# Kernel tuning notes

Measured on AMD Instinct MI355X. Metric: run time of the kernel, lower is better.

## Reference

```python
import jax, jax.numpy as jnp
import numpy as np

N = 50000
E = 800000
D_IN = 128
D_OUT = 128
K = 3


def setup_inputs() -> dict:
    key = jax.random.key(0)
    k1, k2, k3, k4, k5 = jax.random.split(key, 5)
    x = jax.random.normal(k1, (N, D_IN), dtype=jnp.float32)
    TT = jax.random.uniform(k2, (E, K), dtype=jnp.float32)
    weight = jax.random.normal(k3, (D_IN, D_OUT, K), dtype=jnp.float32) * 0.1
    bias = jax.random.normal(k4, (D_OUT,), dtype=jnp.float32) * 0.1
    edge_idx = jax.random.randint(k5, (2, E), 0, N, dtype=jnp.int64)
    return {"x": x, "TT": TT, "weight": weight, "bias": bias, "edge_idx": edge_idx}


def reference(x, TT, weight, bias, edge_idx):
    # out = sum_k A_k @ (x @ W[:, :, k]) + bias, A_k sparse COO with values TT[:, k]
    n = x.shape[0]
    row, col = edge_idx[0], edge_idx[1]
    out = jnp.zeros((n, weight.shape[1]), dtype=x.dtype)
    for k in range(weight.shape[2]):  # small fixed kernel count
        support = x @ weight[:, :, k]                 # [N, out]
        msg = TT[:, k, None] * support[col]           # [E, out] gather + scale
        out = out + jax.ops.segment_sum(msg, row, num_segments=n)
    return out + bias
```

## Files before the change

kernel.cpp:

```cpp
#include <hip/hip_runtime.h>
#include <hip/hip_fp16.h>

#define DIM 128
#define KK 3
#define RPB 16
#define ZPAD 392
#define EBLK 4096
#define NBKT 256
#define CAPB 5120
#define QF   512
#define OVF_CAP 65536

typedef __attribute__((ext_vector_type(4))) float f32x4;
typedef __attribute__((ext_vector_type(8))) short bf16x8;

__device__ __forceinline__ unsigned pkbf(float lo, float hi) {
    unsigned a = __float_as_uint(lo), b = __float_as_uint(hi);
    a = (a + 0x7fffu + ((a >> 16) & 1u)) >> 16;
    b = (b + 0x7fffu + ((b >> 16) & 1u)) & 0xffff0000u;
    return (a & 0xffffu) | b;
}

__global__ __launch_bounds__(256) void k1a_kernel(
        const float* __restrict__ x, const float* __restrict__ w,
        uint2* __restrict__ xb2q, bf16x8* __restrict__ wbf,
        int xq_total, int xblk) {
    int b = blockIdx.x;
    if (b < xblk) {
        int i = b * 256 + threadIdx.x;
        if (i < xq_total) {
            float4 v = ((const float4*)x)[i];
            xb2q[i] = make_uint2(pkbf(v.x, v.y), pkbf(v.z, v.w));
        }
    } else {
        int t = (b - xblk) * 256 + threadIdx.x;
        if (t < 12 * 8 * 64) {
            int lane = t & 63;
            int quad = lane >> 4;
            int nn = ((t >> 6) & 7) * 16 + (lane & 15);
            int kbase = (t >> 9) * 32 + quad * 8;
            short vals[8];
#pragma unroll
            for (int j = 0; j < 8; ++j) {
                int k = kbase + j;
                int k3 = k >> 7, i2 = k & (DIM - 1);
                unsigned bv = __float_as_uint(w[((size_t)i2 * DIM + nn) * KK + k3]);
                vals[j] = (short)((bv + 0x7fffu + ((bv >> 16) & 1u)) >> 16);
            }
            wbf[t] = *(const bf16x8*)vals;
        }
    }
}

__global__ __launch_bounds__(1024) void binA_kernel(
        const float* __restrict__ TT, const int* __restrict__ eidx,
        int* __restrict__ bucketCnt, uint4* __restrict__ rec16,
        int* __restrict__ ovf_cnt, uint4* __restrict__ ovf, int E) {
    __shared__ unsigned sw0[EBLK], sw1[EBLK], sw2[EBLK], sw3[EBLK];
    __shared__ int hist[NBKT], scn[NBKT], cursor[NBKT], gbase[NBKT];
    int tid = threadIdx.x, blk = blockIdx.x;
    int e0 = blk * EBLK;
    int nval = min(EBLK, E - e0);

    if (tid < NBKT) hist[tid] = 0;
    __syncthreads();

    unsigned w0v[4], w1v[4], w2v[4], w3v[4];
    int bv[4];
#pragma unroll
    for (int i = 0; i < 4; ++i) {
        int li = tid + i * 1024;
        bv[i] = -1;
        if (li < nval) {
            int e = e0 + li;
            int row = eidx[e];
            int col = eidx[(size_t)E + e];
            w0v[i] = (unsigned)col | ((unsigned)row << 16);
            w1v[i] = __float_as_uint(TT[(size_t)e * 3 + 0]);
            w2v[i] = __float_as_uint(TT[(size_t)e * 3 + 1]);
            w3v[i] = __float_as_uint(TT[(size_t)e * 3 + 2]);
            bv[i] = row >> 8;
            atomicAdd(&hist[bv[i]], 1);
        }
    }
    __syncthreads();

    if (tid < NBKT) scn[tid] = hist[tid];
    __syncthreads();
    for (int d = 1; d < NBKT; d <<= 1) {
        int v = 0;
        if (tid < NBKT && tid >= d) v = scn[tid - d];
        __syncthreads();
        if (tid < NBKT && tid >= d) scn[tid] += v;
        __syncthreads();
    }
    if (tid < NBKT) {
        int ex = scn[tid] - hist[tid];
        scn[tid] = ex;
        cursor[tid] = ex;
        gbase[tid] = atomicAdd(&bucketCnt[tid], hist[tid]);
    }
    __syncthreads();

#pragma unroll
    for (int i = 0; i < 4; ++i) {
        if (bv[i] >= 0) {
            int lpos = atomicAdd(&cursor[bv[i]], 1);
            sw0[lpos] = w0v[i]; sw1[lpos] = w1v[i];
            sw2[lpos] = w2v[i]; sw3[lpos] = w3v[i];
        }
    }
    __syncthreads();

    for (int s = tid; s < nval; s += 1024) {
        unsigned u0 = sw0[s];
        int bb = (int)(u0 >> 24);
        int gpos = gbase[bb] + (s - scn[bb]);
        if (gpos < CAPB) {
            rec16[(size_t)bb * CAPB + gpos] = make_uint4(u0, sw1[s], sw2[s], sw3[s]);
        } else {
            int op = atomicAdd(ovf_cnt, 1);
            if (op < OVF_CAP)
                ovf[op] = make_uint4(u0, sw1[s], sw2[s], sw3[s]);
        }
    }
}

__global__ __launch_bounds__(1024) void binB_kernel(
        const uint4* __restrict__ rec16, const int* __restrict__ bucketCnt,
        uint4* __restrict__ out16, int* __restrict__ rowStart,
        int* __restrict__ rowCnt) {
    __shared__ uint4 ostage[CAPB];
    __shared__ int hist[256], scn[256], cursor[256];
    int b = blockIdx.x, tid = threadIdx.x;
    int cntb = min(bucketCnt[b], CAPB);

    if (tid < 256) hist[tid] = 0;
    __syncthreads();
    for (int i = tid; i < cntb; i += 1024) {
        unsigned u0 = rec16[(size_t)b * CAPB + i].x;
        atomicAdd(&hist[(u0 >> 16) & 255u], 1);
    }
    __syncthreads();
    if (tid < 256) scn[tid] = hist[tid];
    __syncthreads();
    for (int d = 1; d < 256; d <<= 1) {
        int v = 0;
        if (tid < 256 && tid >= d) v = scn[tid - d];
        __syncthreads();
        if (tid < 256 && tid >= d) scn[tid] += v;
        __syncthreads();
    }
    if (tid < 256) {
        int ex = scn[tid] - hist[tid];
        scn[tid] = ex;
        cursor[tid] = ex;
        rowStart[b * 256 + tid] = b * CAPB + ex;
        rowCnt[b * 256 + tid] = hist[tid];
    }
    __syncthreads();
    for (int i = tid; i < cntb; i += 1024) {
        uint4 r = rec16[(size_t)b * CAPB + i];
        int rl = (int)((r.x >> 16) & 255u);
        int pos = atomicAdd(&cursor[rl], 1);
        ostage[pos] = r;
    }
    __syncthreads();
    for (int i = tid; i < cntb; i += 1024)
        out16[(size_t)b * CAPB + i] = ostage[i];
}

__device__ __forceinline__ void edge_fma(uint4 rc, const unsigned* __restrict__ xb2, int lane,
        float& a0l, float& a0h, float& a1l, float& a1h, float& a2l, float& a2h) {
    int c = rc.x & 0xffffu;
    float t0 = __uint_as_float(rc.y);
    float t1 = __uint_as_float(rc.z);
    float t2 = __uint_as_float(rc.w);
    unsigned u = xb2[(size_t)c * 64 + lane];
    float xl = __uint_as_float(u << 16), xh = __uint_as_float(u & 0xffff0000u);
    a0l = fmaf(t0, xl, a0l); a0h = fmaf(t0, xh, a0h);
    a1l = fmaf(t1, xl, a1l); a1h = fmaf(t1, xh, a1h);
    a2l = fmaf(t2, xl, a2l); a2h = fmaf(t2, xh, a2h);
}

__global__ __launch_bounds__(256) void fused_kernel(const uint4* __restrict__ out16,
        const int* __restrict__ rowStart, const int* __restrict__ rowCnt,
        const unsigned* __restrict__ xb2, const bf16x8* __restrict__ wbf,
        const float* __restrict__ bias, float* __restrict__ out, int n) {
    __shared__ short zs16[RPB][ZPAD];
    __shared__ uint4 qflat[QF];
    __shared__ int rs[RPB], rc[RPB];
    int tid = threadIdx.x;
    int lane = tid & 63, wv = tid >> 6;
    int n0 = blockIdx.x * RPB;

    if (tid < RPB) {
        int r = n0 + tid;
        rs[tid] = (r < n) ? rowStart[r] : 0;
        rc[tid] = (r < n) ? rowCnt[r] : 0;
    }
    __syncthreads();
    int base = rs[0];
    int tot = rs[RPB - 1] + rc[RPB - 1] - base;

    float A[4][6];
#pragma unroll
    for (int ii = 0; ii < 4; ++ii)
#pragma unroll
        for (int j = 0; j < 6; ++j) A[ii][j] = 0.f;

    for (int c0 = 0; c0 < tot; c0 += QF) {
        int cl = min(QF, tot - c0);
        __syncthreads();
        for (int i = tid; i < cl; i += 256) qflat[i] = out16[(size_t)base + c0 + i];
        __syncthreads();
#pragma unroll
        for (int ii = 0; ii < 4; ++ii) {
            int rl = wv * 4 + ii;
            int s = rs[rl] - base, e = s + rc[rl];
            int lo = max(s, c0), hi = min(e, c0 + cl);
            int p = lo;
            for (; p + 8 <= hi; p += 8) {
#pragma unroll
                for (int u8 = 0; u8 < 8; ++u8)
                    edge_fma(qflat[p - c0 + u8], xb2, lane,
                             A[ii][0], A[ii][1], A[ii][2], A[ii][3], A[ii][4], A[ii][5]);
            }
            for (; p + 4 <= hi; p += 4) {
#pragma unroll
                for (int u4 = 0; u4 < 4; ++u4)
                    edge_fma(qflat[p - c0 + u4], xb2, lane,
                             A[ii][0], A[ii][1], A[ii][2], A[ii][3], A[ii][4], A[ii][5]);
            }
            for (; p < hi; ++p)
                edge_fma(qflat[p - c0], xb2, lane,
                         A[ii][0], A[ii][1], A[ii][2], A[ii][3], A[ii][4], A[ii][5]);
        }
    }

#pragma unroll
    for (int ii = 0; ii < 4; ++ii) {
        int rl = wv * 4 + ii;
        *(unsigned*)&zs16[rl][0 * DIM + 2 * lane] = pkbf(A[ii][0], A[ii][1]);
        *(unsigned*)&zs16[rl][1 * DIM + 2 * lane] = pkbf(A[ii][2], A[ii][3]);
        *(unsigned*)&zs16[rl][2 * DIM + 2 * lane] = pkbf(A[ii][4], A[ii][5]);
    }
    __syncthreads();

    int quad = lane >> 4, m = lane & 15;
    int nt0 = wv * 2, nt1 = wv * 2 + 1;
    f32x4 acc0 = {0.f, 0.f, 0.f, 0.f}, acc1 = {0.f, 0.f, 0.f, 0.f};
#pragma unroll
    for (int kt = 0; kt < 12; ++kt) {
        bf16x8 a  = *(const bf16x8*)&zs16[m][kt * 32 + quad * 8];
        bf16x8 b0 = wbf[(kt * 8 + nt0) * 64 + lane];
        bf16x8 b1 = wbf[(kt * 8 + nt1) * 64 + lane];
        acc0 = __builtin_amdgcn_mfma_f32_16x16x32_bf16(a, b0, acc0, 0, 0, 0);
        acc1 = __builtin_amdgcn_mfma_f32_16x16x32_bf16(a, b1, acc1, 0, 0, 0);
    }
    float bi0 = bias[nt0 * 16 + m], bi1 = bias[nt1 * 16 + m];
#pragma unroll
    for (int rr = 0; rr < 4; ++rr) {
        int node = n0 + quad * 4 + rr;
        if (node < n) {
            out[(size_t)node * DIM + nt0 * 16 + m] = acc0[rr] + bi0;
            out[(size_t)node * DIM + nt1 * 16 + m] = acc1[rr] + bi1;
        }
    }
}

__global__ __launch_bounds__(128) void ovf_kernel(const uint4* __restrict__ ovf,
        const int* __restrict__ ovf_cnt, const float* __restrict__ x,
        const float* __restrict__ w, float* __restrict__ out) {
    int total = min(*ovf_cnt, OVF_CAP);
    int d = threadIdx.x;
    for (int i = blockIdx.x; i < total; i += gridDim.x) {
        uint4 r = ovf[i];
        int col = (int)(r.x & 0xffffu), row = (int)(r.x >> 16);
        float t0 = __uint_as_float(r.y);
        float t1 = __uint_as_float(r.z);
        float t2 = __uint_as_float(r.w);
        float acc = 0.f;
        for (int ii = 0; ii < DIM; ++ii) {
            const float* wp = &w[((size_t)ii * DIM + d) * KK];
            acc = fmaf(x[(size_t)col * DIM + ii],
                       t0 * wp[0] + t1 * wp[1] + t2 * wp[2], acc);
        }
        atomicAdd(&out[(size_t)row * DIM + d], acc);
    }
}

extern "C" void kernel_launch(void* const* d_in, const int* in_sizes, int n_in,
                              void* d_out, int out_size, void* d_ws, size_t ws_size,
                              hipStream_t stream) {
    const float* x    = (const float*)d_in[0];
    const float* TT   = (const float*)d_in[1];
    const float* w    = (const float*)d_in[2];
    const float* bias = (const float*)d_in[3];
    const int*   eidx = (const int*)d_in[4];
    float* out = (float*)d_out;

    int n = in_sizes[0] / DIM;
    int E = in_sizes[1] / KK;
    int nbkt = (n + 255) >> 8;

    char* ws = (char*)d_ws;
    size_t o = 0;
    auto take = [&](size_t b) { void* p = ws + o; o += (b + 255) & ~(size_t)255; return p; };
    uint4*    rec16 = (uint4*)take((size_t)nbkt * CAPB * 16);
    uint4*    out16 = (uint4*)take((size_t)nbkt * CAPB * 16);
    int*      rowStart = (int*)take((size_t)nbkt * 256 * 4);
    int*      rowCnt   = (int*)take((size_t)nbkt * 256 * 4);
    int*      bcnt  = (int*)take((size_t)(NBKT + 64) * 4);
    uint4*    ovf   = (uint4*)take((size_t)OVF_CAP * 16);
    bf16x8*   wbf   = (bf16x8*)take((size_t)12 * 8 * 64 * 16);
    unsigned* xb2   = (unsigned*)take((size_t)n * DIM * 2);
    (void)ws_size;
    int* ovf_cnt = bcnt + NBKT;

    hipMemsetAsync(bcnt, 0, (size_t)(NBKT + 64) * 4, stream);

    int xq = n * DIM / 4;
    int xblk = (xq + 255) / 256;
    int ablk = (E + EBLK - 1) / EBLK;

    k1a_kernel<<<xblk + 24, 256, 0, stream>>>(x, w, (uint2*)xb2, wbf, xq, xblk);
    binA_kernel<<<ablk, 1024, 0, stream>>>(TT, eidx, bcnt, rec16, ovf_cnt, ovf, E);
    binB_kernel<<<nbkt, 1024, 0, stream>>>(rec16, bcnt, out16, rowStart, rowCnt);
    fused_kernel<<<(n + RPB - 1) / RPB, 256, 0, stream>>>(
        out16, rowStart, rowCnt, xb2, wbf, bias, out, n);
    ovf_kernel<<<64, 128, 0, stream>>>(ovf, ovf_cnt, x, w, out);
}
```

Measured before the change: 164.1 us.

## Split binB per bucket quarter and make fused kernel persistent with prefetch

binB now launches four blocks per bucket. Each block handles a quarter of the rows, which halves the shared staging buffer and raises parallelism. The fused kernel becomes persistent with a fixed grid, each block processing up to four 16-row tiles. It double-buffers the edge-record loads by prefetching the next tile's records into registers while the current tile is gathered and multiplied. Tiles with more than QF edges now spill their extra records to the overflow path instead of looping, which adds atomics and leaves correctness dependent on the overflow kernel.

```diff
diff --git a/kernel.cpp b/kernel.cpp
--- a/kernel.cpp
+++ b/kernel.cpp
@@ -9,6 +9,9 @@
 #define NBKT 256
 #define CAPB 5120
 #define QF   512
+#define CAPQ 2560
+#define TPB  4
+#define FGRID 1024
 #define OVF_CAP 65536
 
 typedef __attribute__((ext_vector_type(4))) float f32x4;
@@ -130,15 +133,15 @@
         const uint4* __restrict__ rec16, const int* __restrict__ bucketCnt,
         uint4* __restrict__ out16, int* __restrict__ rowStart,
         int* __restrict__ rowCnt) {
-    __shared__ uint4 ostage[CAPB];
-    __shared__ int hist[256], scn[256], cursor[256];
-    int b = blockIdx.x, tid = threadIdx.x;
-    int cntb = min(bucketCnt[b], CAPB);
+    __shared__ uint4 ostage[CAPQ];
+    __shared__ int hist[256], scn[256], cursor[64];
+    int bb = blockIdx.x >> 2, q = blockIdx.x & 3, tid = threadIdx.x;
+    int cntb = min(bucketCnt[bb], CAPB);
 
     if (tid < 256) hist[tid] = 0;
     __syncthreads();
     for (int i = tid; i < cntb; i += 1024) {
-        unsigned u0 = rec16[(size_t)b * CAPB + i].x;
+        unsigned u0 = rec16[(size_t)bb * CAPB + i].x;
         atomicAdd(&hist[(u0 >> 16) & 255u], 1);
     }
     __syncthreads();
@@ -151,23 +154,32 @@
         if (tid < 256 && tid >= d) scn[tid] += v;
         __syncthreads();
     }
+    int r0 = q * 64;
     if (tid < 256) {
         int ex = scn[tid] - hist[tid];
         scn[tid] = ex;
-        cursor[tid] = ex;
-        rowStart[b * 256 + tid] = b * CAPB + ex;
-        rowCnt[b * 256 + tid] = hist[tid];
-    }
+        if ((tid >> 6) == q) {
+            rowStart[bb * 256 + tid] = bb * CAPB + ex;
+            rowCnt[bb * 256 + tid] = hist[tid];
+        }
+    }
+    __syncthreads();
+    int qbase = scn[r0];
+    int qend = (q == 3) ? cntb : scn[r0 + 64];
+    if (tid < 64) cursor[tid] = scn[r0 + tid] - qbase;
     __syncthreads();
     for (int i = tid; i < cntb; i += 1024) {
-        uint4 r = rec16[(size_t)b * CAPB + i];
-        int rl = (int)((r.x >> 16) & 255u);
-        int pos = atomicAdd(&cursor[rl], 1);
-        ostage[pos] = r;
-    }
-    __syncthreads();
-    for (int i = tid; i < cntb; i += 1024)
-        out16[(size_t)b * CAPB + i] = ostage[i];
+        uint4 r = rec16[(size_t)bb * CAPB + i];
+        int rr = (int)((r.x >> 16) & 255u);
+        if ((rr >> 6) == q) {
+            int pos = atomicAdd(&cursor[rr - r0], 1);
+            if (pos < CAPQ) ostage[pos] = r;
+        }
+    }
+    __syncthreads();
+    int qcnt = min(qend - qbase, CAPQ);
+    for (int i = tid; i < qcnt; i += 1024)
+        out16[(size_t)bb * CAPB + qbase + i] = ostage[i];
 }
 
 __device__ __forceinline__ void edge_fma(uint4 rc, const unsigned* __restrict__ xb2, int lane,
@@ -186,86 +198,116 @@
 __global__ __launch_bounds__(256) void fused_kernel(const uint4* __restrict__ out16,
         const int* __restrict__ rowStart, const int* __restrict__ rowCnt,
         const unsigned* __restrict__ xb2, const bf16x8* __restrict__ wbf,
-        const float* __restrict__ bias, float* __restrict__ out, int n) {
+        const float* __restrict__ bias, float* __restrict__ out,
+        int* __restrict__ ovf_cnt, uint4* __restrict__ ovf,
+        int n, int ntiles) {
     __shared__ short zs16[RPB][ZPAD];
-    __shared__ uint4 qflat[QF];
-    __shared__ int rs[RPB], rc[RPB];
+    __shared__ uint4 qbuf[2][QF];
+    __shared__ int rsL[TPB][RPB], rcL[TPB][RPB];
     int tid = threadIdx.x;
     int lane = tid & 63, wv = tid >> 6;
-    int n0 = blockIdx.x * RPB;
+    int bid = blockIdx.x;
 
     if (tid < RPB) {
-        int r = n0 + tid;
-        rs[tid] = (r < n) ? rowStart[r] : 0;
-        rc[tid] = (r < n) ? rowCnt[r] : 0;
-    }
-    __syncthreads();
-    int base = rs[0];
-    int tot = rs[RPB - 1] + rc[RPB - 1] - base;
-
-    float A[4][6];
-#pragma unroll
-    for (int ii = 0; ii < 4; ++ii)
-#pragma unroll
-        for (int j = 0; j < 6; ++j) A[ii][j] = 0.f;
-
-    for (int c0 = 0; c0 < tot; c0 += QF) {
-        int cl = min(QF, tot - c0);
-        __syncthreads();
-        for (int i = tid; i < cl; i += 256) qflat[i] = out16[(size_t)base + c0 + i];
-        __syncthreads();
+#pragma unroll
+        for (int k = 0; k < TPB; ++k) {
+            int tt = bid + k * FGRID;
+            if (tt < ntiles) {
+                int r = tt * RPB + tid;
+                rsL[k][tid] = (r < n) ? rowStart[r] : 0;
+                rcL[k][tid] = (r < n) ? rowCnt[r] : 0;
+            }
+        }
+    }
+    __syncthreads();
+
+    {
+        int base0 = rsL[0][0];
+        int raw0 = rsL[0][RPB - 1] + rcL[0][RPB - 1] - base0;
+        for (int i = tid; i < raw0; i += 256) {
+            uint4 r = out16[(size_t)base0 + i];
+            if (i < QF) qbuf[0][i] = r;
+            else {
+                int op = atomicAdd(ovf_cnt, 1);
+                if (op < OVF_CAP) ovf[op] = r;
+            }
+        }
+    }
+    __syncthreads();
+
+    int quad = lane >> 4, m = lane & 15;
+    int nt0 = wv * 2, nt1 = wv * 2 + 1;
+    float bi0 = bias[nt0 * 16 + m], bi1 = bias[nt1 * 16 + m];
+    int buf = 0;
+
+    for (int k = 0; k < TPB && (bid + k * FGRID) < ntiles; ++k) {
+        int n0 = (bid + k * FGRID) * RPB;
+        int base = rsL[k][0];
+
+        bool hasn = (k + 1 < TPB) && (bid + (k + 1) * FGRID) < ntiles;
+        uint4 pf0, pf1; int ntot = 0;
+        if (hasn) {
+            int nbase = rsL[k + 1][0];
+            int rawn = rsL[k + 1][RPB - 1] + rcL[k + 1][RPB - 1] - nbase;
+            ntot = min(rawn, QF);
+            if (tid < ntot) pf0 = out16[(size_t)nbase + tid];
+            if (256 + tid < ntot) pf1 = out16[(size_t)nbase + 256 + tid];
+            for (int i = QF + tid; i < rawn; i += 256) {
+                int op = atomicAdd(ovf_cnt, 1);
+                if (op < OVF_CAP) ovf[op] = out16[(size_t)nbase + i];
+            }
+        }
+
+        const uint4* qf = qbuf[buf];
 #pragma unroll
         for (int ii = 0; ii < 4; ++ii) {
             int rl = wv * 4 + ii;
-            int s = rs[rl] - base, e = s + rc[rl];
-            int lo = max(s, c0), hi = min(e, c0 + cl);
-            int p = lo;
-            for (; p + 8 <= hi; p += 8) {
-#pragma unroll
-                for (int u8 = 0; u8 < 8; ++u8)
-                    edge_fma(qflat[p - c0 + u8], xb2, lane,
-                             A[ii][0], A[ii][1], A[ii][2], A[ii][3], A[ii][4], A[ii][5]);
+            float a0l = 0, a0h = 0, a1l = 0, a1h = 0, a2l = 0, a2h = 0;
+            int s = rsL[k][rl] - base;
+            int hi = min(s + rcL[k][rl], QF);
+            int p = min(s, QF);
+            for (; p + 16 <= hi; p += 16) {
+#pragma unroll
+                for (int u = 0; u < 16; ++u)
+                    edge_fma(qf[p + u], xb2, lane, a0l, a0h, a1l, a1h, a2l, a2h);
             }
             for (; p + 4 <= hi; p += 4) {
 #pragma unroll
-                for (int u4 = 0; u4 < 4; ++u4)
-                    edge_fma(qflat[p - c0 + u4], xb2, lane,
-                             A[ii][0], A[ii][1], A[ii][2], A[ii][3], A[ii][4], A[ii][5]);
+                for (int u = 0; u < 4; ++u)
+                    edge_fma(qf[p + u], xb2, lane, a0l, a0h, a1l, a1h, a2l, a2h);
             }
             for (; p < hi; ++p)
-                edge_fma(qflat[p - c0], xb2, lane,
-                         A[ii][0], A[ii][1], A[ii][2], A[ii][3], A[ii][4], A[ii][5]);
-        }
-    }
-
-#pragma unroll
-    for (int ii = 0; ii < 4; ++ii) {
-        int rl = wv * 4 + ii;
-        *(unsigned*)&zs16[rl][0 * DIM + 2 * lane] = pkbf(A[ii][0], A[ii][1]);
-        *(unsigned*)&zs16[rl][1 * DIM + 2 * lane] = pkbf(A[ii][2], A[ii][3]);
-        *(unsigned*)&zs16[rl][2 * DIM + 2 * lane] = pkbf(A[ii][4], A[ii][5]);
-    }
-    __syncthreads();
-
-    int quad = lane >> 4, m = lane & 15;
-    int nt0 = wv * 2, nt1 = wv * 2 + 1;
-    f32x4 acc0 = {0.f, 0.f, 0.f, 0.f}, acc1 = {0.f, 0.f, 0.f, 0.f};
-#pragma unroll
-    for (int kt = 0; kt < 12; ++kt) {
-        bf16x8 a  = *(const bf16x8*)&zs16[m][kt * 32 + quad * 8];
-        bf16x8 b0 = wbf[(kt * 8 + nt0) * 64 + lane];
-        bf16x8 b1 = wbf[(kt * 8 + nt1) * 64 + lane];
-        acc0 = __builtin_amdgcn_mfma_f32_16x16x32_bf16(a, b0, acc0, 0, 0, 0);
-        acc1 = __builtin_amdgcn_mfma_f32_16x16x32_bf16(a, b1, acc1, 0, 0, 0);
-    }
-    float bi0 = bias[nt0 * 16 + m], bi1 = bias[nt1 * 16 + m];
-#pragma unroll
-    for (int rr = 0; rr < 4; ++rr) {
-        int node = n0 + quad * 4 + rr;
-        if (node < n) {
-            out[(size_t)node * DIM + nt0 * 16 + m] = acc0[rr] + bi0;
-            out[(size_t)node * DIM + nt1 * 16 + m] = acc1[rr] + bi1;
-        }
+                edge_fma(qf[p], xb2, lane, a0l, a0h, a1l, a1h, a2l, a2h);
+            *(unsigned*)&zs16[rl][0 * DIM + 2 * lane] = pkbf(a0l, a0h);
+            *(unsigned*)&zs16[rl][1 * DIM + 2 * lane] = pkbf(a1l, a1h);
+            *(unsigned*)&zs16[rl][2 * DIM + 2 * lane] = pkbf(a2l, a2h);
+        }
+        __syncthreads();
+
+        f32x4 acc0 = {0.f, 0.f, 0.f, 0.f}, acc1 = {0.f, 0.f, 0.f, 0.f};
+#pragma unroll
+        for (int kt = 0; kt < 12; ++kt) {
+            bf16x8 a  = *(const bf16x8*)&zs16[m][kt * 32 + quad * 8];
+            bf16x8 b0 = wbf[(kt * 8 + nt0) * 64 + lane];
+            bf16x8 b1 = wbf[(kt * 8 + nt1) * 64 + lane];
+            acc0 = __builtin_amdgcn_mfma_f32_16x16x32_bf16(a, b0, acc0, 0, 0, 0);
+            acc1 = __builtin_amdgcn_mfma_f32_16x16x32_bf16(a, b1, acc1, 0, 0, 0);
+        }
+#pragma unroll
+        for (int rr = 0; rr < 4; ++rr) {
+            int node = n0 + quad * 4 + rr;
+            if (node < n) {
+                out[(size_t)node * DIM + nt0 * 16 + m] = acc0[rr] + bi0;
+                out[(size_t)node * DIM + nt1 * 16 + m] = acc1[rr] + bi1;
+            }
+        }
+
+        if (hasn) {
+            if (tid < ntot) qbuf[buf ^ 1][tid] = pf0;
+            if (256 + tid < ntot) qbuf[buf ^ 1][256 + tid] = pf1;
+        }
+        __syncthreads();
+        buf ^= 1;
     }
 }
 
@@ -303,12 +345,13 @@
     int n = in_sizes[0] / DIM;
     int E = in_sizes[1] / KK;
     int nbkt = (n + 255) >> 8;
+    int ntiles = (n + RPB - 1) / RPB;
 
     char* ws = (char*)d_ws;
     size_t o = 0;
     auto take = [&](size_t b) { void* p = ws + o; o += (b + 255) & ~(size_t)255; return p; };
     uint4*    rec16 = (uint4*)take((size_t)nbkt * CAPB * 16);
-    uint4*    out16 = (uint4*)take((size_t)nbkt * CAPB * 16);
+    uint4*    out16 = (uint4*)take((size_t)nbkt * CAPB * 16 + 8192);
     int*      rowStart = (int*)take((size_t)nbkt * 256 * 4);
     int*      rowCnt   = (int*)take((size_t)nbkt * 256 * 4);
     int*      bcnt  = (int*)take((size_t)(NBKT + 64) * 4);
@@ -326,8 +369,8 @@
 
     k1a_kernel<<<xblk + 24, 256, 0, stream>>>(x, w, (uint2*)xb2, wbf, xq, xblk);
     binA_kernel<<<ablk, 1024, 0, stream>>>(TT, eidx, bcnt, rec16, ovf_cnt, ovf, E);
-    binB_kernel<<<nbkt, 1024, 0, stream>>>(rec16, bcnt, out16, rowStart, rowCnt);
-    fused_kernel<<<(n + RPB - 1) / RPB, 256, 0, stream>>>(
-        out16, rowStart, rowCnt, xb2, wbf, bias, out, n);
+    binB_kernel<<<nbkt * 4, 1024, 0, stream>>>(rec16, bcnt, out16, rowStart, rowCnt);
+    fused_kernel<<<FGRID, 256, 0, stream>>>(
+        out16, rowStart, rowCnt, xb2, wbf, bias, out, ovf_cnt, ovf, n, ntiles);
     ovf_kernel<<<64, 128, 0, stream>>>(ovf, ovf_cnt, x, w, out);
 }
```

Result: slower. 244.9 us (+49.2%).

## Merge prep and binning kernels; single-chunk gather with overflow spill in fused kernel

Applied to the files above, without the earlier changes.

Folds the bf16 conversion, weight packing and edge-binning (binA) work into one 1024-thread launch, which removes a kernel launch and its boundary. The fused kernel now stages at most QF edge records per 16-row tile in shared memory. Any excess records are pushed to the global overflow list with an atomic, so ovf_kernel handles them instead of running a multi-chunk loop. This makes the gather loop simpler, but the x/w conversion blocks now carry the large shared-memory footprint of the binning path, which may reduce their occupancy. Correctness also depends on the overflow buffer being large enough.

```diff
diff --git a/kernel.cpp b/kernel.cpp
--- a/kernel.cpp
+++ b/kernel.cpp
@@ -21,19 +21,27 @@
     return (a & 0xffffu) | b;
 }
 
-__global__ __launch_bounds__(256) void k1a_kernel(
+__global__ __launch_bounds__(1024) void prep_kernel(
         const float* __restrict__ x, const float* __restrict__ w,
+        const float* __restrict__ TT, const int* __restrict__ eidx,
         uint2* __restrict__ xb2q, bf16x8* __restrict__ wbf,
-        int xq_total, int xblk) {
-    int b = blockIdx.x;
+        int* __restrict__ bucketCnt, uint4* __restrict__ rec16,
+        int* __restrict__ ovf_cnt, uint4* __restrict__ ovf,
+        int xq_total, int xblk, int E) {
+    __shared__ unsigned sw0[EBLK], sw1[EBLK], sw2[EBLK], sw3[EBLK];
+    __shared__ int hist[NBKT], scn[NBKT], cursor[NBKT], gbase[NBKT];
+    int tid = threadIdx.x, b = blockIdx.x;
+
     if (b < xblk) {
-        int i = b * 256 + threadIdx.x;
+        int i = b * 1024 + tid;
         if (i < xq_total) {
             float4 v = ((const float4*)x)[i];
             xb2q[i] = make_uint2(pkbf(v.x, v.y), pkbf(v.z, v.w));
         }
-    } else {
-        int t = (b - xblk) * 256 + threadIdx.x;
+        return;
+    }
+    if (b < xblk + 6) {
+        int t = (b - xblk) * 1024 + tid;
         if (t < 12 * 8 * 64) {
             int lane = t & 63;
             int quad = lane >> 4;
@@ -49,17 +57,10 @@
             }
             wbf[t] = *(const bf16x8*)vals;
         }
-    }
-}
-
-__global__ __launch_bounds__(1024) void binA_kernel(
-        const float* __restrict__ TT, const int* __restrict__ eidx,
-        int* __restrict__ bucketCnt, uint4* __restrict__ rec16,
-        int* __restrict__ ovf_cnt, uint4* __restrict__ ovf, int E) {
-    __shared__ unsigned sw0[EBLK], sw1[EBLK], sw2[EBLK], sw3[EBLK];
-    __shared__ int hist[NBKT], scn[NBKT], cursor[NBKT], gbase[NBKT];
-    int tid = threadIdx.x, blk = blockIdx.x;
-    int e0 = blk * EBLK;
+        return;
+    }
+
+    int e0 = (b - xblk - 6) * EBLK;
     int nval = min(EBLK, E - e0);
 
     if (tid < NBKT) hist[tid] = 0;
@@ -186,7 +187,8 @@
 __global__ __launch_bounds__(256) void fused_kernel(const uint4* __restrict__ out16,
         const int* __restrict__ rowStart, const int* __restrict__ rowCnt,
         const unsigned* __restrict__ xb2, const bf16x8* __restrict__ wbf,
-        const float* __restrict__ bias, float* __restrict__ out, int n) {
+        const float* __restrict__ bias, float* __restrict__ out,
+        int* __restrict__ ovf_cnt, uint4* __restrict__ ovf, int n) {
     __shared__ short zs16[RPB][ZPAD];
     __shared__ uint4 qflat[QF];
     __shared__ int rs[RPB], rc[RPB];
@@ -203,47 +205,35 @@
     int base = rs[0];
     int tot = rs[RPB - 1] + rc[RPB - 1] - base;
 
-    float A[4][6];
-#pragma unroll
-    for (int ii = 0; ii < 4; ++ii)
-#pragma unroll
-        for (int j = 0; j < 6; ++j) A[ii][j] = 0.f;
-
-    for (int c0 = 0; c0 < tot; c0 += QF) {
-        int cl = min(QF, tot - c0);
-        __syncthreads();
-        for (int i = tid; i < cl; i += 256) qflat[i] = out16[(size_t)base + c0 + i];
-        __syncthreads();
-#pragma unroll
-        for (int ii = 0; ii < 4; ++ii) {
-            int rl = wv * 4 + ii;
-            int s = rs[rl] - base, e = s + rc[rl];
-            int lo = max(s, c0), hi = min(e, c0 + cl);
-            int p = lo;
-            for (; p + 8 <= hi; p += 8) {
-#pragma unroll
-                for (int u8 = 0; u8 < 8; ++u8)
-                    edge_fma(qflat[p - c0 + u8], xb2, lane,
-                             A[ii][0], A[ii][1], A[ii][2], A[ii][3], A[ii][4], A[ii][5]);
-            }
-            for (; p + 4 <= hi; p += 4) {
-#pragma unroll
-                for (int u4 = 0; u4 < 4; ++u4)
-                    edge_fma(qflat[p - c0 + u4], xb2, lane,
-                             A[ii][0], A[ii][1], A[ii][2], A[ii][3], A[ii][4], A[ii][5]);
-            }
-            for (; p < hi; ++p)
-                edge_fma(qflat[p - c0], xb2, lane,
-                         A[ii][0], A[ii][1], A[ii][2], A[ii][3], A[ii][4], A[ii][5]);
-        }
-    }
+    for (int i = tid; i < tot; i += 256) {
+        uint4 r = out16[(size_t)base + i];
+        if (i < QF) qflat[i] = r;
+        else {
+            int op = atomicAdd(ovf_cnt, 1);
+            if (op < OVF_CAP) ovf[op] = r;
+        }
+    }
+    __syncthreads();
 
 #pragma unroll
     for (int ii = 0; ii < 4; ++ii) {
         int rl = wv * 4 + ii;
-        *(unsigned*)&zs16[rl][0 * DIM + 2 * lane] = pkbf(A[ii][0], A[ii][1]);
-        *(unsigned*)&zs16[rl][1 * DIM + 2 * lane] = pkbf(A[ii][2], A[ii][3]);
-        *(unsigned*)&zs16[rl][2 * DIM + 2 * lane] = pkbf(A[ii][4], A[ii][5]);
+        float a0l = 0, a0h = 0, a1l = 0, a1h = 0, a2l = 0, a2h = 0;
+        int s = min(rs[rl] - base, QF);
+        int hi = min(rs[rl] - base + rc[rl], QF);
+        int p = s;
+        for (; p + 4 <= hi; p += 4) {
+            uint4 r0 = qflat[p], r1 = qflat[p + 1], r2 = qflat[p + 2], r3 = qflat[p + 3];
+            edge_fma(r0, xb2, lane, a0l, a0h, a1l, a1h, a2l, a2h);
+            edge_fma(r1, xb2, lane, a0l, a0h, a1l, a1h, a2l, a2h);
+            edge_fma(r2, xb2, lane, a0l, a0h, a1l, a1h, a2l, a2h);
+            edge_fma(r3, xb2, lane, a0l, a0h, a1l, a1h, a2l, a2h);
+        }
+        for (; p < hi; ++p)
+            edge_fma(qflat[p], xb2, lane, a0l, a0h, a1l, a1h, a2l, a2h);
+        *(unsigned*)&zs16[rl][0 * DIM + 2 * lane] = pkbf(a0l, a0h);
+        *(unsigned*)&zs16[rl][1 * DIM + 2 * lane] = pkbf(a1l, a1h);
+        *(unsigned*)&zs16[rl][2 * DIM + 2 * lane] = pkbf(a2l, a2h);
     }
     __syncthreads();
 
@@ -303,6 +293,7 @@
     int n = in_sizes[0] / DIM;
     int E = in_sizes[1] / KK;
     int nbkt = (n + 255) >> 8;
+    int ntiles = (n + RPB - 1) / RPB;
 
     char* ws = (char*)d_ws;
     size_t o = 0;
@@ -321,13 +312,13 @@
     hipMemsetAsync(bcnt, 0, (size_t)(NBKT + 64) * 4, stream);
 
     int xq = n * DIM / 4;
-    int xblk = (xq + 255) / 256;
+    int xblk = (xq + 1023) / 1024;
     int ablk = (E + EBLK - 1) / EBLK;
 
-    k1a_kernel<<<xblk + 24, 256, 0, stream>>>(x, w, (uint2*)xb2, wbf, xq, xblk);
-    binA_kernel<<<ablk, 1024, 0, stream>>>(TT, eidx, bcnt, rec16, ovf_cnt, ovf, E);
+    prep_kernel<<<xblk + 6 + ablk, 1024, 0, stream>>>(
+        x, w, TT, eidx, (uint2*)xb2, wbf, bcnt, rec16, ovf_cnt, ovf, xq, xblk, E);
     binB_kernel<<<nbkt, 1024, 0, stream>>>(rec16, bcnt, out16, rowStart, rowCnt);
-    fused_kernel<<<(n + RPB - 1) / RPB, 256, 0, stream>>>(
-        out16, rowStart, rowCnt, xb2, wbf, bias, out, n);
+    fused_kernel<<<ntiles, 256, 0, stream>>>(
+        out16, rowStart, rowCnt, xb2, wbf, bias, out, ovf_cnt, ovf, n);
     ovf_kernel<<<64, 128, 0, stream>>>(ovf, ovf_cnt, x, w, out);
 }
```

Measured after the change: 153.4 us. 1.07x faster.
